# Optimization experiments

Measured on AMD Instinct MI355X. Metric: run time of the kernel, lower is better.

The kernel has to match this reference:

```python
import jax, jax.numpy as jnp
import numpy as np

B, S, D = 2, 2048, 2048
H, HKV = 16, 4
HD = D // H  # 128
ROPE_BASE = 10000.0


def _rope(t, cos, sin):
    # t: [B, h, S, HD]; torch variant: x1 = even dims, x2 = odd dims,
    # output = concat([x1*cos - x2*sin, x1*sin + x2*cos], axis=-1)
    x1 = t[..., ::2]
    x2 = t[..., 1::2]
    return jnp.concatenate([x1 * cos - x2 * sin, x1 * sin + x2 * cos], axis=-1)


def setup_inputs() -> dict:
    key = jax.random.key(0)
    kx, kq, kk, kv, ko = jax.random.split(key, 5)
    x = jax.random.normal(kx, (B, S, D), dtype=jnp.float32)
    scale = 0.02
    Wq = jax.random.normal(kq, (D, H * HD), dtype=jnp.float32) * scale
    Wk = jax.random.normal(kk, (D, HKV * HD), dtype=jnp.float32) * scale
    Wv = jax.random.normal(kv, (D, HKV * HD), dtype=jnp.float32) * scale
    Wo = jax.random.normal(ko, (H * HD, D), dtype=jnp.float32) * scale
    mask = jnp.tril(jnp.ones((S, S), dtype=bool))  # causal
    return {"x": x, "Wq": Wq, "Wk": Wk, "Wv": Wv, "Wo": Wo, "mask": mask}


def reference(x, Wq, Wk, Wv, Wo, mask):
    b, s, d = x.shape
    # projections: [B,S,h,HD] -> [B,h,S,HD]
    q = (x @ Wq).reshape(b, s, H, HD).transpose(0, 2, 1, 3)
    k = (x @ Wk).reshape(b, s, HKV, HD).transpose(0, 2, 1, 3)
    v = (x @ Wv).reshape(b, s, HKV, HD).transpose(0, 2, 1, 3)

    # RoPE tables: [S, HD/2]
    theta = 1.0 / (ROPE_BASE ** (jnp.arange(0, HD, 2, dtype=jnp.float32) / HD))
    angles = jnp.arange(s, dtype=jnp.float32)[:, None] * theta
    cos, sin = jnp.cos(angles), jnp.sin(angles)

    q = _rope(q, cos, sin)
    k = _rope(k, cos, sin)

    # GQA: repeat_interleave kv heads along head dim
    rep = H // HKV
    k = jnp.repeat(k, rep, axis=1)
    v = jnp.repeat(v, rep, axis=1)

    scores = jnp.einsum("bhqd,bhkd->bhqk", q, k) / jnp.sqrt(jnp.float32(HD))
    scores = jnp.where(mask, scores, -jnp.inf)
    attn = jax.nn.softmax(scores, axis=-1)

    out = jnp.einsum("bhqk,bhkd->bqhd", attn, v).reshape(b, s, H * HD)
    return out @ Wo
```

## Files before the change

kernel.cpp:

```cpp
#include <hip/hip_runtime.h>

typedef __bf16 bf16;
typedef __bf16 bf16x8 __attribute__((ext_vector_type(8)));
typedef float f32x4 __attribute__((ext_vector_type(4)));
typedef short s16x4 __attribute__((ext_vector_type(4)));

#define B_ 2
#define S_ 2048
#define D_ 2048
#define H_ 16
#define HKV_ 4
#define HD_ 128
#define QKVW 3072
#define QKW 2560
#define SCALE 0.08838834764831845f
#define NEGINF -30000.0f

__device__ inline void gload16(const void* g, void* l) {
  __builtin_amdgcn_global_load_lds((const __attribute__((address_space(1))) unsigned int*)g,
                                   (__attribute__((address_space(3))) unsigned int*)l, 16, 0, 0);
}

__device__ inline unsigned short bfb(float v) {
  union { bf16 h; unsigned short u; } c;
  c.h = (bf16)v;
  return c.u;
}

__global__ void detect_dtype(const unsigned* __restrict__ xw, int* __restrict__ flag) {
  __shared__ int cnt;
  if (threadIdx.x == 0) cnt = 0;
  __syncthreads();
  unsigned w = xw[(size_t)threadIdx.x * 16384];
  unsigned low = w & 0xFFFFu;
  int e = (int)((low >> 7) & 0xFF);
  int vote = (low == 0u || (e >= 100 && e <= 140)) ? 1 : 0;
  atomicAdd(&cnt, vote);
  __syncthreads();
  if (threadIdx.x == 0) *flag = (cnt >= 128) ? 1 : 0;
}

__global__ __launch_bounds__(256) void cast_x(const void* __restrict__ x,
                                              bf16* __restrict__ out,
                                              const int* __restrict__ flag) {
  int fm = *flag;
  long i = ((long)blockIdx.x * 256 + threadIdx.x) << 3;
  if (fm) {
    *(uint4*)(out + i) = *(const uint4*)((const bf16*)x + i);
  } else {
    const float* fp = (const float*)x + i;
    float4 a = *(const float4*)fp, b = *(const float4*)(fp + 4);
    alignas(16) bf16 t[8];
    t[0] = (bf16)a.x; t[1] = (bf16)a.y; t[2] = (bf16)a.z; t[3] = (bf16)a.w;
    t[4] = (bf16)b.x; t[5] = (bf16)b.y; t[6] = (bf16)b.z; t[7] = (bf16)b.w;
    *(uint4*)(out + i) = *(uint4*)t;
  }
}

__global__ __launch_bounds__(256) void transpose_qkvw(
    const void* __restrict__ Wq, const void* __restrict__ Wk, const void* __restrict__ Wv,
    bf16* __restrict__ wqkvT, const int* __restrict__ flag) {
  int z = blockIdx.z;
  const void* in = (z == 0) ? Wq : (z == 1) ? Wk : Wv;
  int cols = (z == 0) ? 2048 : 512;
  bf16* out = wqkvT + ((z == 0) ? 0 : (z == 1) ? 2048 * 2048 : 2560 * 2048);
  if (blockIdx.x * 32 >= cols) return;
  int fm = *flag;
  __shared__ float tile[32][33];
  int c0 = blockIdx.x * 32, r0 = blockIdx.y * 32;
  int tx = threadIdx.x, ty = threadIdx.y;
#pragma unroll
  for (int i = 0; i < 32; i += 8) {
    long idx = (long)(r0 + ty + i) * cols + c0 + tx;
    tile[ty + i][tx] = fm ? (float)((const bf16*)in)[idx] : ((const float*)in)[idx];
  }
  __syncthreads();
#pragma unroll
  for (int i = 0; i < 32; i += 8)
    out[(long)(c0 + ty + i) * 2048 + r0 + tx] = (bf16)tile[tx][ty + i];
}

__global__ __launch_bounds__(256) void transpose_cvt(
    const void* __restrict__ in, bf16* __restrict__ out,
    long in_stride, long out_stride, const int* __restrict__ flag) {
  __shared__ float tile[32][33];
  int fm = *flag;
  int c0 = blockIdx.x * 32, r0 = blockIdx.y * 32;
  int tx = threadIdx.x, ty = threadIdx.y;
#pragma unroll
  for (int i = 0; i < 32; i += 8) {
    long idx = (long)(r0 + ty + i) * in_stride + c0 + tx;
    tile[ty + i][tx] = fm ? (float)((const bf16*)in)[idx] : ((const float*)in)[idx];
  }
  __syncthreads();
#pragma unroll
  for (int i = 0; i < 32; i += 8)
    out[(long)(c0 + ty + i) * out_stride + r0 + tx] = (bf16)tile[tx][ty + i];
}

#define BM 128
#define BN 128
#define BK 32

__global__ __launch_bounds__(256) void gemm_bt(
    const void* __restrict__ A, const bf16* __restrict__ Bt, void* __restrict__ C,
    int M, int N, int K, int ldc, int ncmax,
    bf16* __restrict__ vt_out, int vcol0,
    const int* __restrict__ flag, int adyn, int cdyn) {
  alignas(16) __shared__ bf16 la[2 * BM * BK];
  alignas(16) __shared__ bf16 lb[2 * BN * BK];
  int fm = flag ? *flag : 1;
  bool af32 = adyn && !fm;
  bool cf32 = cdyn && !fm;
  int tid = threadIdx.x;
  int wave = tid >> 6, lane = tid & 63;
  int wr = wave >> 1, wc = wave & 1;
  int quad = lane >> 4, l16 = lane & 15;

  int nwg = (int)(gridDim.x * gridDim.y);
  int flat = (int)(blockIdx.y * gridDim.x + blockIdx.x);
  int cpx = nwg >> 3;
  int wk = (flat & 7) * cpx + (flat >> 3);
  int bx = wk % (int)gridDim.x, by = wk / (int)gridDim.x;
  int m0 = by * BM, n0 = bx * BN;

  f32x4 acc[4][4] = {};

  int sr = (wave << 4) + (lane >> 2);
  int sc = (((lane & 3) - (sr >> 1)) & 3) << 3;
  const bf16* gb0 = Bt + (long)(n0 + sr) * K + sc;
  const bf16* gb1 = Bt + (long)(n0 + 64 + sr) * K + sc;
  int lo0 = (wave << 9);
  int lo1 = 2048 + (wave << 9);
  const bf16* ga0 = nullptr; const bf16* ga1 = nullptr;
  const float* gaf = nullptr;
  int fr = tid >> 1, fh = (tid & 1) << 4;
  if (af32) gaf = (const float*)A + (long)(m0 + fr) * K + fh;
  else { ga0 = (const bf16*)A + (long)(m0 + sr) * K + sc;
         ga1 = (const bf16*)A + (long)(m0 + 64 + sr) * K + sc; }
  int c0 = fh >> 3;
  int k2 = (fr >> 1) & 3;
  int ws0 = ((c0 + k2) & 3) << 3;
  int ws1 = ((c0 + 1 + k2) & 3) << 3;

  int nk = K / BK;

  auto cvtwrite = [&](const float4* f, int buf) {
    alignas(16) bf16 tt[16];
#pragma unroll
    for (int u = 0; u < 4; u++) {
      tt[4 * u] = (bf16)f[u].x; tt[4 * u + 1] = (bf16)f[u].y;
      tt[4 * u + 2] = (bf16)f[u].z; tt[4 * u + 3] = (bf16)f[u].w;
    }
    bf16* rowp = la + (buf << 12) + fr * BK;
    *(uint4*)(rowp + ws0) = *(uint4*)tt;
    *(uint4*)(rowp + ws1) = *(uint4*)(tt + 8);
  };
  auto compute = [&](int buf) {
    const bf16* baA = la + (buf << 12);
    const bf16* baB = lb + (buf << 12);
    bf16x8 afr[4], bfr[4];
#pragma unroll
    for (int i = 0; i < 4; i++) {
      int rowA = (wr << 6) + (i << 4) + l16;
      afr[i] = *(const bf16x8*)(baA + rowA * BK + (((quad + (rowA >> 1)) & 3) << 3));
    }
#pragma unroll
    for (int j = 0; j < 4; j++) {
      int rowB = (wc << 6) + (j << 4) + l16;
      bfr[j] = *(const bf16x8*)(baB + rowB * BK + (((quad + (rowB >> 1)) & 3) << 3));
    }
#pragma unroll
    for (int i = 0; i < 4; i++)
#pragma unroll
      for (int j = 0; j < 4; j++)
        acc[i][j] = __builtin_amdgcn_mfma_f32_16x16x32_bf16(afr[i], bfr[j], acc[i][j], 0, 0, 0);
  };

  gload16(gb0, lb + lo0);
  gload16(gb1, lb + lo1);
  if (af32) {
    float4 f0[4];
#pragma unroll
    for (int u = 0; u < 4; u++) f0[u] = *(const float4*)(gaf + 4 * u);
    cvtwrite(f0, 0);
  } else {
    gload16(ga0, la + lo0);
    gload16(ga1, la + lo1);
  }
  __syncthreads();

  for (int t = 0; t < nk; ++t) {
    int cur = t & 1, nxt = cur ^ 1;
    bool hasnext = (t + 1 < nk);
    float4 f[4];
    if (hasnext) {
      int k0 = (t + 1) * BK;
      gload16(gb0 + k0, lb + (nxt << 12) + lo0);
      gload16(gb1 + k0, lb + (nxt << 12) + lo1);
      if (af32) {
        const float* fp = gaf + k0;
#pragma unroll
        for (int u = 0; u < 4; u++) f[u] = *(const float4*)(fp + 4 * u);
      } else {
        gload16(ga0 + k0, la + (nxt << 12) + lo0);
        gload16(ga1 + k0, la + (nxt << 12) + lo1);
      }
    }

    compute(cur);

    if (hasnext && af32) cvtwrite(f, nxt);
    __syncthreads();
  }

  if (vt_out && n0 >= vcol0) {
#pragma unroll
    for (int i = 0; i < 4; i++)
#pragma unroll
      for (int j = 0; j < 4; j++) {
        int col = n0 + (wc << 6) + (j << 4) + l16;
        int hdg = col - vcol0;
        int row0 = m0 + (wr << 6) + (i << 4) + (quad << 2);
        int bb = row0 >> 11, s = row0 & 2047;
        ushort4 p;
        p.x = bfb(acc[i][j][0]); p.y = bfb(acc[i][j][1]);
        p.z = bfb(acc[i][j][2]); p.w = bfb(acc[i][j][3]);
        *(ushort4*)(vt_out + (((long)(bb * 512 + hdg)) << 11) + s) = p;
      }
  } else {
#pragma unroll
    for (int i = 0; i < 4; i++)
#pragma unroll
      for (int j = 0; j < 4; j++) {
        int col = n0 + (wc << 6) + (j << 4) + l16;
        if (col >= ncmax) continue;
#pragma unroll
        for (int r = 0; r < 4; r++) {
          long row = m0 + (wr << 6) + (i << 4) + (quad << 2) + r;
          float v = acc[i][j][r];
          if (cf32) ((float*)C)[row * ldc + col] = v;
          else      ((bf16*)C)[row * ldc + col] = (bf16)v;
        }
      }
  }
}

#define WBM 128
#define WBN 256
#define WBK 32

__global__ __launch_bounds__(512, 4) void gemm_bt_wide(
    const void* __restrict__ A, const bf16* __restrict__ Bt, bf16* __restrict__ C,
    int K, int ldc, int ncmax,
    bf16* __restrict__ vt_out, int vcol0, const int* __restrict__ flag) {
  alignas(16) __shared__ bf16 la[2 * WBM * WBK];
  alignas(16) __shared__ bf16 lb[2 * WBN * WBK];
  int fm = flag ? *flag : 1;
  bool af32 = !fm;
  int tid = threadIdx.x;
  int wave = tid >> 6, lane = tid & 63;
  int wm = wave >> 2, wn = wave & 3;
  int quad = lane >> 4, l16 = lane & 15;

  int nwg = (int)(gridDim.x * gridDim.y);
  int flat = (int)(blockIdx.y * gridDim.x + blockIdx.x);
  int cpx = nwg >> 3;
  int wk = (flat & 7) * cpx + (flat >> 3);
  int bx = wk % (int)gridDim.x, by = wk / (int)gridDim.x;
  int m0 = by * WBM, n0 = bx * WBN;

  f32x4 acc[4][4] = {};

  const bf16* gb[2];
  int lbo[2];
#pragma unroll
  for (int u = 0; u < 2; u++) {
    int sr2 = (wave << 5) + (u << 4) + (lane >> 2);
    int sc2 = (((lane & 3) - (sr2 >> 1)) & 3) << 3;
    gb[u] = Bt + (long)(n0 + sr2) * K + sc2;
    lbo[u] = ((wave << 5) + (u << 4)) << 5;
  }
  const bf16* gaB = nullptr;
  const float* gaf = nullptr;
  int lao = (wave << 4) << 5;
  int fr = tid >> 2, fc = tid & 3;
  int wso = 0;
  if (af32) {
    gaf = (const float*)A + (long)(m0 + fr) * K + (fc << 3);
    wso = (fr << 5) + ((((fc) + (fr >> 1)) & 3) << 3);
  } else {
    int ra = (wave << 4) + (lane >> 2);
    int sca = (((lane & 3) - (ra >> 1)) & 3) << 3;
    gaB = (const bf16*)A + (long)(m0 + ra) * K + sca;
  }

  int nk = K / WBK;

  auto cvtwrite = [&](const float4* f, int buf) {
    alignas(16) bf16 tt[8];
    tt[0] = (bf16)f[0].x; tt[1] = (bf16)f[0].y; tt[2] = (bf16)f[0].z; tt[3] = (bf16)f[0].w;
    tt[4] = (bf16)f[1].x; tt[5] = (bf16)f[1].y; tt[6] = (bf16)f[1].z; tt[7] = (bf16)f[1].w;
    *(uint4*)(la + (buf << 12) + wso) = *(uint4*)tt;
  };
  auto compute = [&](int buf) {
    const bf16* baA = la + (buf << 12);
    const bf16* baB = lb + (buf << 13);
    bf16x8 afr[4], bfr[4];
#pragma unroll
    for (int i = 0; i < 4; i++) {
      int rowA = (wm << 6) + (i << 4) + l16;
      afr[i] = *(const bf16x8*)(baA + (rowA << 5) + (((quad + (rowA >> 1)) & 3) << 3));
    }
#pragma unroll
    for (int j = 0; j < 4; j++) {
      int rowB = (wn << 6) + (j << 4) + l16;
      bfr[j] = *(const bf16x8*)(baB + (rowB << 5) + (((quad + (rowB >> 1)) & 3) << 3));
    }
#pragma unroll
    for (int i = 0; i < 4; i++)
#pragma unroll
      for (int j = 0; j < 4; j++)
        acc[i][j] = __builtin_amdgcn_mfma_f32_16x16x32_bf16(afr[i], bfr[j], acc[i][j], 0, 0, 0);
  };

  gload16(gb[0], lb + lbo[0]);
  gload16(gb[1], lb + lbo[1]);
  if (af32) {
    float4 f0[2];
    f0[0] = *(const float4*)gaf;
    f0[1] = *(const float4*)(gaf + 4);
    cvtwrite(f0, 0);
  } else {
    gload16(gaB, la + lao);
  }
  __syncthreads();

  for (int t = 0; t < nk; ++t) {
    int cur = t & 1, nxt = cur ^ 1;
    bool hasnext = (t + 1 < nk);
    float4 f[2];
    if (hasnext) {
      int k0 = (t + 1) * WBK;
      gload16(gb[0] + k0, lb + (nxt << 13) + lbo[0]);
      gload16(gb[1] + k0, lb + (nxt << 13) + lbo[1]);
      if (af32) {
        f[0] = *(const float4*)(gaf + k0);
        f[1] = *(const float4*)(gaf + k0 + 4);
      } else {
        gload16(gaB + k0, la + (nxt << 12) + lao);
      }
    }

    compute(cur);

    if (hasnext && af32) cvtwrite(f, nxt);
    __syncthreads();
  }

  if (vt_out && n0 >= vcol0) {
#pragma unroll
    for (int i = 0; i < 4; i++)
#pragma unroll
      for (int j = 0; j < 4; j++) {
        int col = n0 + (wn << 6) + (j << 4) + l16;
        int hdg = col - vcol0;
        int row0 = m0 + (wm << 6) + (i << 4) + (quad << 2);
        int bb = row0 >> 11, s = row0 & 2047;
        ushort4 p;
        p.x = bfb(acc[i][j][0]); p.y = bfb(acc[i][j][1]);
        p.z = bfb(acc[i][j][2]); p.w = bfb(acc[i][j][3]);
        *(ushort4*)(vt_out + (((long)(bb * 512 + hdg)) << 11) + s) = p;
      }
  } else {
#pragma unroll
    for (int i = 0; i < 4; i++)
#pragma unroll
      for (int j = 0; j < 4; j++) {
        int col = n0 + (wn << 6) + (j << 4) + l16;
        if (col >= ncmax) continue;
#pragma unroll
        for (int r = 0; r < 4; r++) {
          long row = m0 + (wm << 6) + (i << 4) + (quad << 2) + r;
          C[row * ldc + col] = (bf16)acc[i][j][r];
        }
      }
  }
}

__global__ __launch_bounds__(256) void rope_scatter(
    const bf16* __restrict__ qkv, bf16* __restrict__ Q, bf16* __restrict__ Ko) {
  int row = blockIdx.x;
  int b = row >> 11, s = row & 2047;
  int tid = threadIdx.x;
  int i = tid & 63;
  const bf16* src = qkv + (long)row * QKW;
  float theta = __expf(-0.14391156831212787f * (float)i);
  float sn, cs;
  sincosf((float)s * theta, &sn, &cs);
#pragma unroll
  for (int it = 0; it < 4; ++it) {
    int h = (tid + it * 256) >> 6;
    unsigned v = *(const unsigned*)(src + h * 128 + 2 * i);
    float x1 = __uint_as_float(v << 16);
    float x2 = __uint_as_float(v & 0xFFFF0000u);
    long qb = ((long)(b * H_ + h) * S_ + s) * HD_;
    Q[qb + i]      = (bf16)((x1 * cs - x2 * sn) * SCALE);
    Q[qb + 64 + i] = (bf16)((x1 * sn + x2 * cs) * SCALE);
  }
  {
    int kh = tid >> 6;
    unsigned v = *(const unsigned*)(src + 2048 + kh * 128 + 2 * i);
    float x1 = __uint_as_float(v << 16);
    float x2 = __uint_as_float(v & 0xFFFF0000u);
    long kb = ((long)(b * HKV_ + kh) * S_ + s) * HD_;
    Ko[kb + i]      = (bf16)(x1 * cs - x2 * sn);
    Ko[kb + 64 + i] = (bf16)(x1 * sn + x2 * cs);
  }
}

#define KTILE 8192
#define VTILE 8192

__global__ __launch_bounds__(256) void attn_kernel(
    const bf16* __restrict__ Q, const bf16* __restrict__ K,
    const bf16* __restrict__ Vt, bf16* __restrict__ O) {
  alignas(16) __shared__ bf16 Ks[2 * KTILE];
  alignas(16) __shared__ bf16 Vs[2 * VTILE];
  int bi = (int)blockIdx.x;
  int cb = bi & 7;
  int b = cb >> 2, kh = cb & 3;
  int r = bi >> 3;
  int qt0 = r >> 2;
  int h = kh * 4 + (r & 3);
  int tid = threadIdx.x, wave = tid >> 6, lane = tid & 63;
  int quad = lane >> 4, l16 = lane & 15;
  const bf16* Kg = K + ((long)(b * HKV_ + kh) * S_) * HD_;
  const bf16* Vg = Vt + ((long)(b * HKV_ + kh) * HD_) * S_;

  int kgo[4], vgo[4], klo[4], vlo[4];
#pragma unroll
  for (int u = 0; u < 4; u++) {
    int i = u * 4 + wave;
    int rr = i * 4 + quad;
    int c = l16 ^ (rr & 15);
    kgo[u] = rr * HD_ + c * 8;
    klo[u] = i * 512;
    int v = i * 8 + (lane >> 3);
    int cv = (lane & 7) ^ (v & 7);
    vgo[u] = v * S_ + cv * 8;
    vlo[u] = i * 512;
  }

  for (int hf = 0; hf < 2; ++hf) {
    int qt = hf ? 31 - qt0 : qt0;
    int q0 = qt * 64;
    const bf16* Qg = Q + ((long)(b * H_ + h) * S_ + q0) * HD_;

    bf16x8 qb[4];
    {
      const bf16* qrow = Qg + (wave * 16 + l16) * HD_ + quad * 8;
#pragma unroll
      for (int kk = 0; kk < 4; kk++) qb[kk] = *(const bf16x8*)(qrow + kk * 32);
    }

    if (hf) __syncthreads();

#pragma unroll
    for (int u = 0; u < 4; u++) {
      gload16(Kg + kgo[u], Ks + klo[u]);
      gload16(Vg + vgo[u], Vs + vlo[u]);
    }

    f32x4 Of[8] = {};
    float m_run = NEGINF, l_run = 0.f;

    for (int kt = 0; kt <= qt; ++kt) {
      __syncthreads();
      int p = kt & 1;
      if (kt < qt) {
        const bf16* kn = Kg + (long)(kt + 1) * 8192;
        const bf16* vn = Vg + (long)(kt + 1) * 64;
        bf16* kd = Ks + (p ^ 1) * KTILE;
        bf16* vd = Vs + (p ^ 1) * VTILE;
#pragma unroll
        for (int u = 0; u < 4; u++) {
          gload16(kn + kgo[u], kd + klo[u]);
          gload16(vn + vgo[u], vd + vlo[u]);
        }
      }
      const bf16* kc = Ks + p * KTILE;
      const bf16* vc = Vs + p * VTILE;

      bool diag = (kt == qt);
      f32x4 sf[4];
      __builtin_amdgcn_s_setprio(1);
#pragma unroll
      for (int jb = 0; jb < 4; jb++) {
        if (diag && jb > wave) {
          sf[jb] = (f32x4){NEGINF, NEGINF, NEGINF, NEGINF};
        } else {
          f32x4 a = {};
          const bf16* kbase = kc + (jb * 16 + l16) * 128;
#pragma unroll
          for (int kk = 0; kk < 4; kk++) {
            bf16x8 kf = *(const bf16x8*)(kbase + (((kk * 4 + quad) ^ l16) * 8));
            a = __builtin_amdgcn_mfma_f32_16x16x32_bf16(kf, qb[kk], a, 0, 0, 0);
          }
          sf[jb] = a;
        }
      }
      __builtin_amdgcn_s_setprio(0);
      if (diag) {
#pragma unroll
        for (int jb = 0; jb < 4; jb++)
          if (jb == wave) {
#pragma unroll
            for (int r2 = 0; r2 < 4; r2++)
              if (quad * 4 + r2 > l16) sf[jb][r2] = NEGINF;
          }
      }

      float mx = NEGINF;
#pragma unroll
      for (int jb = 0; jb < 4; jb++)
#pragma unroll
        for (int r2 = 0; r2 < 4; r2++) mx = fmaxf(mx, sf[jb][r2]);
      mx = fmaxf(mx, __shfl_xor(mx, 16));
      mx = fmaxf(mx, __shfl_xor(mx, 32));
      if (__any(mx > m_run + 8.0f)) {
        float mnew = fmaxf(m_run, mx);
        float alpha = __expf(m_run - mnew);
        m_run = mnew;
        l_run *= alpha;
#pragma unroll
        for (int n = 0; n < 8; n++) Of[n] *= alpha;
      }

      float ls = 0.f;
      s16x4 pk[4];
#pragma unroll
      for (int jb = 0; jb < 4; jb++) {
        float p0 = __expf(sf[jb][0] - m_run);
        float p1 = __expf(sf[jb][1] - m_run);
        float p2 = __expf(sf[jb][2] - m_run);
        float p3 = __expf(sf[jb][3] - m_run);
        ls += (p0 + p1) + (p2 + p3);
        s16x4 t;
        t.x = (short)bfb(p0); t.y = (short)bfb(p1);
        t.z = (short)bfb(p2); t.w = (short)bfb(p3);
        pk[jb] = t;
      }
      l_run += ls;

      __builtin_amdgcn_s_setprio(1);
#pragma unroll
      for (int jb = 0; jb < 4; jb++) {
        if (diag && jb > wave) continue;
#pragma unroll
        for (int n = 0; n < 8; n++) {
          int v = n * 16 + l16;
          const bf16* va_p = vc + v * 64 + (((jb * 2 + (quad >> 1)) ^ (l16 & 7)) * 8) + (quad & 1) * 4;
          s16x4 va = *(const s16x4*)va_p;
          Of[n] = __builtin_amdgcn_mfma_f32_16x16x16bf16_1k(va, pk[jb], Of[n], 0, 0, 0);
        }
      }
      __builtin_amdgcn_s_setprio(0);
    }

    l_run += __shfl_xor(l_run, 16);
    l_run += __shfl_xor(l_run, 32);
    float inv = 1.0f / fmaxf(l_run, 1e-30f);
    bf16* Ob = O + ((long)(b * S_) + q0 + wave * 16 + l16) * D_ + h * HD_;
#pragma unroll
    for (int n = 0; n < 8; n++) {
      ushort4 w;
      w.x = bfb(Of[n][0] * inv); w.y = bfb(Of[n][1] * inv);
      w.z = bfb(Of[n][2] * inv); w.w = bfb(Of[n][3] * inv);
      *(ushort4*)(Ob + n * 16 + quad * 4) = w;
    }
  }
}

extern "C" void kernel_launch(void* const* d_in, const int* in_sizes, int n_in,
                              void* d_out, int out_size, void* d_ws, size_t ws_size,
                              hipStream_t stream) {
  const void* x  = d_in[0];
  const void* Wq = d_in[1];
  const void* Wk = d_in[2];
  const void* Wv = d_in[3];
  const void* Wo = d_in[4];
  bf16* ws = (bf16*)d_ws;
  int* flag = (int*)d_ws;

  bf16* qkv   = ws + 16;
  bf16* Vtb   = ws + 10485776;
  bf16* Qb    = ws + 12582928;
  bf16* wqkvT = ws + 12582928;
  bf16* Kb    = ws + 20971536;
  bf16* attno = ws + 16;
  bf16* woT   = ws + 10485776;
  bf16* xb    = (bf16*)d_out;

  dim3 tb(32, 8);
  detect_dtype<<<1, 256, 0, stream>>>((const unsigned*)x, flag);
  cast_x<<<4096, 256, 0, stream>>>(x, xb, flag);
  transpose_qkvw<<<dim3(64, 64, 3), tb, 0, stream>>>(Wq, Wk, Wv, wqkvT, flag);
  gemm_bt_wide<<<dim3(QKVW / WBN, (B_ * S_) / WBM), 512, 0, stream>>>(
      xb, wqkvT, qkv, D_, QKW, QKW, Vtb, QKW, nullptr);
  rope_scatter<<<B_ * S_, 256, 0, stream>>>(qkv, Qb, Kb);
  attn_kernel<<<dim3(512, 1, 1), 256, 0, stream>>>(Qb, Kb, Vtb, attno);
  transpose_cvt<<<dim3(64, 64, 1), tb, 0, stream>>>(Wo, woT, 2048, 2048, flag);
  gemm_bt<<<dim3(D_ / BN, (B_ * S_) / BM), 256, 0, stream>>>(
      attno, woT, d_out, B_ * S_, D_, D_, D_, D_, nullptr, 0, flag, 0, 1);
}
```

Before: 370.0 us.

## Split attention blocks per query tile and read V directly from global

Each attention block now handles a single 64-row query tile instead of a paired early/late tile, doubling the grid to 1024 blocks and ordering tiles to interleave short and long causal rows. V is no longer staged in LDS; the PV MFMA operands are loaded straight from the transposed V in global memory, halving LDS use, and launch bounds request 4 blocks per CU. This aims to raise occupancy and cut LDS traffic and barriers, at the cost of uncoalesced global V loads that depend on cache hits and weaker load balance per block.

```diff
diff --git a/kernel.cpp b/kernel.cpp
--- a/kernel.cpp
+++ b/kernel.cpp
@@ -420,25 +420,26 @@
 }
 
 #define KTILE 8192
-#define VTILE 8192
-
-__global__ __launch_bounds__(256) void attn_kernel(
+
+__global__ __launch_bounds__(256, 4) void attn_kernel(
     const bf16* __restrict__ Q, const bf16* __restrict__ K,
     const bf16* __restrict__ Vt, bf16* __restrict__ O) {
   alignas(16) __shared__ bf16 Ks[2 * KTILE];
-  alignas(16) __shared__ bf16 Vs[2 * VTILE];
   int bi = (int)blockIdx.x;
   int cb = bi & 7;
   int b = cb >> 2, kh = cb & 3;
   int r = bi >> 3;
-  int qt0 = r >> 2;
   int h = kh * 4 + (r & 3);
+  int j = r >> 2;
+  int lo = j & 7, hi = j >> 3;
+  int qt = (hi == 0) ? lo : (hi == 1) ? 15 - lo : (hi == 2) ? 16 + lo : 31 - lo;
+  int q0 = qt * 64;
   int tid = threadIdx.x, wave = tid >> 6, lane = tid & 63;
   int quad = lane >> 4, l16 = lane & 15;
   const bf16* Kg = K + ((long)(b * HKV_ + kh) * S_) * HD_;
   const bf16* Vg = Vt + ((long)(b * HKV_ + kh) * HD_) * S_;
 
-  int kgo[4], vgo[4], klo[4], vlo[4];
+  int kgo[4], klo[4];
 #pragma unroll
   for (int u = 0; u < 4; u++) {
     int i = u * 4 + wave;
@@ -446,139 +447,123 @@
     int c = l16 ^ (rr & 15);
     kgo[u] = rr * HD_ + c * 8;
     klo[u] = i * 512;
-    int v = i * 8 + (lane >> 3);
-    int cv = (lane & 7) ^ (v & 7);
-    vgo[u] = v * S_ + cv * 8;
-    vlo[u] = i * 512;
-  }
-
-  for (int hf = 0; hf < 2; ++hf) {
-    int qt = hf ? 31 - qt0 : qt0;
-    int q0 = qt * 64;
-    const bf16* Qg = Q + ((long)(b * H_ + h) * S_ + q0) * HD_;
-
-    bf16x8 qb[4];
+  }
+
+  const bf16* Qg = Q + ((long)(b * H_ + h) * S_ + q0) * HD_;
+  bf16x8 qb[4];
+  {
+    const bf16* qrow = Qg + (wave * 16 + l16) * HD_ + quad * 8;
+#pragma unroll
+    for (int kk = 0; kk < 4; kk++) qb[kk] = *(const bf16x8*)(qrow + kk * 32);
+  }
+
+#pragma unroll
+  for (int u = 0; u < 4; u++) gload16(Kg + kgo[u], Ks + klo[u]);
+
+  const bf16* vrow = Vg + (long)l16 * S_ + quad * 4;
+
+  f32x4 Of[8] = {};
+  float m_run = NEGINF, l_run = 0.f;
+
+  for (int kt = 0; kt <= qt; ++kt) {
+    __syncthreads();
+    int p = kt & 1;
+    if (kt < qt) {
+      const bf16* kn = Kg + (long)(kt + 1) * 8192;
+      bf16* kd = Ks + (p ^ 1) * KTILE;
+#pragma unroll
+      for (int u = 0; u < 4; u++) gload16(kn + kgo[u], kd + klo[u]);
+    }
+    const bf16* kc = Ks + p * KTILE;
+
+    bool diag = (kt == qt);
+    f32x4 sf[4];
+    __builtin_amdgcn_s_setprio(1);
+#pragma unroll
+    for (int jb = 0; jb < 4; jb++) {
+      if (diag && jb > wave) {
+        sf[jb] = (f32x4){NEGINF, NEGINF, NEGINF, NEGINF};
+      } else {
+        f32x4 a = {};
+        const bf16* kbase = kc + (jb * 16 + l16) * 128;
+#pragma unroll
+        for (int kk = 0; kk < 4; kk++) {
+          bf16x8 kf = *(const bf16x8*)(kbase + (((kk * 4 + quad) ^ l16) * 8));
+          a = __builtin_amdgcn_mfma_f32_16x16x32_bf16(kf, qb[kk], a, 0, 0, 0);
+        }
+        sf[jb] = a;
+      }
+    }
+    __builtin_amdgcn_s_setprio(0);
+    if (diag) {
+#pragma unroll
+      for (int jb = 0; jb < 4; jb++)
+        if (jb == wave) {
+#pragma unroll
+          for (int r2 = 0; r2 < 4; r2++)
+            if (quad * 4 + r2 > l16) sf[jb][r2] = NEGINF;
+        }
+    }
+
+    float mx = NEGINF;
+#pragma unroll
+    for (int jb = 0; jb < 4; jb++)
+#pragma unroll
+      for (int r2 = 0; r2 < 4; r2++) mx = fmaxf(mx, sf[jb][r2]);
+    mx = fmaxf(mx, __shfl_xor(mx, 16));
+    mx = fmaxf(mx, __shfl_xor(mx, 32));
+    if (__any(mx > m_run + 8.0f)) {
+      float mnew = fmaxf(m_run, mx);
+      float alpha = __expf(m_run - mnew);
+      m_run = mnew;
+      l_run *= alpha;
+#pragma unroll
+      for (int n = 0; n < 8; n++) Of[n] *= alpha;
+    }
+
+    float ls = 0.f;
+    s16x4 pk[4];
+#pragma unroll
+    for (int jb = 0; jb < 4; jb++) {
+      float p0 = __expf(sf[jb][0] - m_run);
+      float p1 = __expf(sf[jb][1] - m_run);
+      float p2 = __expf(sf[jb][2] - m_run);
+      float p3 = __expf(sf[jb][3] - m_run);
+      ls += (p0 + p1) + (p2 + p3);
+      s16x4 t;
+      t.x = (short)bfb(p0); t.y = (short)bfb(p1);
+      t.z = (short)bfb(p2); t.w = (short)bfb(p3);
+      pk[jb] = t;
+    }
+    l_run += ls;
+
+    __builtin_amdgcn_s_setprio(1);
     {
-      const bf16* qrow = Qg + (wave * 16 + l16) * HD_ + quad * 8;
-#pragma unroll
-      for (int kk = 0; kk < 4; kk++) qb[kk] = *(const bf16x8*)(qrow + kk * 32);
-    }
-
-    if (hf) __syncthreads();
-
-#pragma unroll
-    for (int u = 0; u < 4; u++) {
-      gload16(Kg + kgo[u], Ks + klo[u]);
-      gload16(Vg + vgo[u], Vs + vlo[u]);
-    }
-
-    f32x4 Of[8] = {};
-    float m_run = NEGINF, l_run = 0.f;
-
-    for (int kt = 0; kt <= qt; ++kt) {
-      __syncthreads();
-      int p = kt & 1;
-      if (kt < qt) {
-        const bf16* kn = Kg + (long)(kt + 1) * 8192;
-        const bf16* vn = Vg + (long)(kt + 1) * 64;
-        bf16* kd = Ks + (p ^ 1) * KTILE;
-        bf16* vd = Vs + (p ^ 1) * VTILE;
-#pragma unroll
-        for (int u = 0; u < 4; u++) {
-          gload16(kn + kgo[u], kd + klo[u]);
-          gload16(vn + vgo[u], vd + vlo[u]);
-        }
-      }
-      const bf16* kc = Ks + p * KTILE;
-      const bf16* vc = Vs + p * VTILE;
-
-      bool diag = (kt == qt);
-      f32x4 sf[4];
-      __builtin_amdgcn_s_setprio(1);
-#pragma unroll
-      for (int jb = 0; jb < 4; jb++) {
-        if (diag && jb > wave) {
-          sf[jb] = (f32x4){NEGINF, NEGINF, NEGINF, NEGINF};
-        } else {
-          f32x4 a = {};
-          const bf16* kbase = kc + (jb * 16 + l16) * 128;
-#pragma unroll
-          for (int kk = 0; kk < 4; kk++) {
-            bf16x8 kf = *(const bf16x8*)(kbase + (((kk * 4 + quad) ^ l16) * 8));
-            a = __builtin_amdgcn_mfma_f32_16x16x32_bf16(kf, qb[kk], a, 0, 0, 0);
-          }
-          sf[jb] = a;
-        }
-      }
-      __builtin_amdgcn_s_setprio(0);
-      if (diag) {
-#pragma unroll
-        for (int jb = 0; jb < 4; jb++)
-          if (jb == wave) {
-#pragma unroll
-            for (int r2 = 0; r2 < 4; r2++)
-              if (quad * 4 + r2 > l16) sf[jb][r2] = NEGINF;
-          }
-      }
-
-      float mx = NEGINF;
-#pragma unroll
-      for (int jb = 0; jb < 4; jb++)
-#pragma unroll
-        for (int r2 = 0; r2 < 4; r2++) mx = fmaxf(mx, sf[jb][r2]);
-      mx = fmaxf(mx, __shfl_xor(mx, 16));
-      mx = fmaxf(mx, __shfl_xor(mx, 32));
-      if (__any(mx > m_run + 8.0f)) {
-        float mnew = fmaxf(m_run, mx);
-        float alpha = __expf(m_run - mnew);
-        m_run = mnew;
-        l_run *= alpha;
-#pragma unroll
-        for (int n = 0; n < 8; n++) Of[n] *= alpha;
-      }
-
-      float ls = 0.f;
-      s16x4 pk[4];
-#pragma unroll
-      for (int jb = 0; jb < 4; jb++) {
-        float p0 = __expf(sf[jb][0] - m_run);
-        float p1 = __expf(sf[jb][1] - m_run);
-        float p2 = __expf(sf[jb][2] - m_run);
-        float p3 = __expf(sf[jb][3] - m_run);
-        ls += (p0 + p1) + (p2 + p3);
-        s16x4 t;
-        t.x = (short)bfb(p0); t.y = (short)bfb(p1);
-        t.z = (short)bfb(p2); t.w = (short)bfb(p3);
-        pk[jb] = t;
-      }
-      l_run += ls;
-
-      __builtin_amdgcn_s_setprio(1);
-#pragma unroll
-      for (int jb = 0; jb < 4; jb++) {
-        if (diag && jb > wave) continue;
-#pragma unroll
-        for (int n = 0; n < 8; n++) {
-          int v = n * 16 + l16;
-          const bf16* va_p = vc + v * 64 + (((jb * 2 + (quad >> 1)) ^ (l16 & 7)) * 8) + (quad & 1) * 4;
-          s16x4 va = *(const s16x4*)va_p;
+      const bf16* vb = vrow + kt * 64;
+#pragma unroll
+      for (int n = 0; n < 8; n++) {
+        const bf16* vn = vb + (long)(n * 16) * S_;
+#pragma unroll
+        for (int jb = 0; jb < 4; jb++) {
+          if (diag && jb > wave) continue;
+          s16x4 va = *(const s16x4*)(vn + jb * 16);
           Of[n] = __builtin_amdgcn_mfma_f32_16x16x16bf16_1k(va, pk[jb], Of[n], 0, 0, 0);
         }
       }
-      __builtin_amdgcn_s_setprio(0);
-    }
-
-    l_run += __shfl_xor(l_run, 16);
-    l_run += __shfl_xor(l_run, 32);
-    float inv = 1.0f / fmaxf(l_run, 1e-30f);
-    bf16* Ob = O + ((long)(b * S_) + q0 + wave * 16 + l16) * D_ + h * HD_;
-#pragma unroll
-    for (int n = 0; n < 8; n++) {
-      ushort4 w;
-      w.x = bfb(Of[n][0] * inv); w.y = bfb(Of[n][1] * inv);
-      w.z = bfb(Of[n][2] * inv); w.w = bfb(Of[n][3] * inv);
-      *(ushort4*)(Ob + n * 16 + quad * 4) = w;
-    }
+    }
+    __builtin_amdgcn_s_setprio(0);
+  }
+
+  l_run += __shfl_xor(l_run, 16);
+  l_run += __shfl_xor(l_run, 32);
+  float inv = 1.0f / fmaxf(l_run, 1e-30f);
+  bf16* Ob = O + ((long)(b * S_) + q0 + wave * 16 + l16) * D_ + h * HD_;
+#pragma unroll
+  for (int n = 0; n < 8; n++) {
+    ushort4 w;
+    w.x = bfb(Of[n][0] * inv); w.y = bfb(Of[n][1] * inv);
+    w.z = bfb(Of[n][2] * inv); w.w = bfb(Of[n][3] * inv);
+    *(ushort4*)(Ob + n * 16 + quad * 4) = w;
   }
 }
 
@@ -609,7 +594,7 @@
   gemm_bt_wide<<<dim3(QKVW / WBN, (B_ * S_) / WBM), 512, 0, stream>>>(
       xb, wqkvT, qkv, D_, QKW, QKW, Vtb, QKW, nullptr);
   rope_scatter<<<B_ * S_, 256, 0, stream>>>(qkv, Qb, Kb);
-  attn_kernel<<<dim3(512, 1, 1), 256, 0, stream>>>(Qb, Kb, Vtb, attno);
+  attn_kernel<<<dim3(1024, 1, 1), 256, 0, stream>>>(Qb, Kb, Vtb, attno);
   transpose_cvt<<<dim3(64, 64, 1), tb, 0, stream>>>(Wo, woT, 2048, 2048, flag);
   gemm_bt<<<dim3(D_ / BN, (B_ * S_) / BM), 256, 0, stream>>>(
       attno, woT, d_out, B_ * S_, D_, D_, D_, D_, nullptr, 0, flag, 0, 1);
```

Measured after the change: 562.1 us. 51.9% more time.
